# Kernel tuning notes

Measured on AMD Instinct MI355X. Metric: run time of the kernel, lower is better.

Reference implementation:

```python
import jax, jax.numpy as jnp
import numpy as np

NUM_DIHEDRALS = 3
# Idealized backbone geometry (picometers / radians), as in RGN/pNeRF.
BOND_LENGTHS = np.array([145.801, 152.326, 132.868], dtype=np.float32)  # N-CA, CA-C, C-N
BOND_ANGLES = np.array([2.124, 1.941, 2.028], dtype=np.float32)


def setup_inputs() -> dict:
    key = jax.random.key(0)
    num_steps, batch = 2048, 512
    flat_dihedrals = jax.random.uniform(
        key, (num_steps * batch, NUM_DIHEDRALS),
        minval=-np.pi, maxval=np.pi, dtype=jnp.float32)
    return {"flat_dihedrals": flat_dihedrals, "batch_size": batch}


def _l2_normalize(v, eps=1e-12):
    return v / jnp.sqrt(jnp.sum(v * v, axis=-1, keepdims=True) + eps)


def dihedral_to_point(dihedral):
    # dihedral: [L, B, 3] -> points in local frames: [3L, B, 3]
    r_cos_theta = np.float32(BOND_LENGTHS * np.cos(np.pi - BOND_ANGLES))  # [3]
    r_sin_theta = np.float32(BOND_LENGTHS * np.sin(np.pi - BOND_ANGLES))  # [3]
    L, B, _ = dihedral.shape
    pt_x = jnp.broadcast_to(jnp.asarray(r_cos_theta), (L, B, NUM_DIHEDRALS))
    pt_y = jnp.cos(dihedral) * r_sin_theta
    pt_z = jnp.sin(dihedral) * r_sin_theta
    point = jnp.stack([pt_x, pt_y, pt_z], axis=-1)      # [L, B, 3, 3]
    return point.reshape(L * NUM_DIHEDRALS, B, 3)       # [3L, B, 3]


def point_to_coordinate(points):
    # points: [N, B, 3]; sequential NeRF rigid-body chain extension.
    B = points.shape[1]
    init = np.array([[-np.sqrt(0.5), np.sqrt(1.5), 0.0],
                     [-np.sqrt(2.0), 0.0, 0.0],
                     [0.0, 0.0, 0.0]], dtype=np.float32)
    a = jnp.broadcast_to(jnp.asarray(init[0]), (B, 3))
    b = jnp.broadcast_to(jnp.asarray(init[1]), (B, 3))
    c = jnp.broadcast_to(jnp.asarray(init[2]), (B, 3))

    def step(carry, p):
        a, b, c = carry
        bc = _l2_normalize(c - b)                      # [B, 3]
        n = _l2_normalize(jnp.cross(b - a, bc))        # [B, 3]
        # Rotation matrix with columns [bc, n x bc, n]
        m = jnp.stack([bc, jnp.cross(n, bc), n], axis=-1)   # [B, 3, 3]
        coord = jnp.einsum('bij,bj->bi', m, p) + c          # [B, 3]
        return (b, c, coord), coord

    _, coords = jax.lax.scan(step, (a, b, c), points)
    return coords  # [N, B, 3]


def reference(flat_dihedrals, batch_size):
    num_steps = flat_dihedrals.shape[0] // batch_size
    dihedrals = flat_dihedrals.reshape(num_steps, batch_size, NUM_DIHEDRALS)
    points = dihedral_to_point(dihedrals)
    coordinates = point_to_coordinate(points)
    return coordinates
```

## Files before the change

kernel.cpp:

```cpp
#include <hip/hip_runtime.h>
#include <math.h>

#define BATCH 512
#define FRAGS 256
#define GROUP 16
#define NGRP  (FRAGS/GROUP)
#define BTILE 32
#define NTILE (BATCH/BTILE)
#define RPF   8
#define READY 0x5EADBEEF

__device__ __forceinline__ void compose(const float* A, const float* B, float* D) {
    float d[12];
    #pragma unroll
    for (int i = 0; i < 3; ++i) {
        #pragma unroll
        for (int j = 0; j < 3; ++j)
            d[i*3+j] = A[i*3+0]*B[0*3+j] + A[i*3+1]*B[1*3+j] + A[i*3+2]*B[2*3+j];
        d[9+i] = A[i*3+0]*B[9] + A[i*3+1]*B[10] + A[i*3+2]*B[11] + A[9+i];
    }
    #pragma unroll
    for (int k = 0; k < 12; ++k) D[k] = d[k];
}

__device__ __forceinline__ void set_identity(float* D) {
    D[0]=1.f; D[1]=0.f; D[2]=0.f;
    D[3]=0.f; D[4]=1.f; D[5]=0.f;
    D[6]=0.f; D[7]=0.f; D[8]=1.f;
    D[9]=0.f; D[10]=0.f; D[11]=0.f;
}

__device__ __forceinline__ void frame_of(
    float ax, float ay, float az,
    float bx, float by, float bz,
    float cx, float cy, float cz,
    float* out )
{
    float bcx = cx - bx, bcy = cy - by, bcz = cz - bz;
    float inv = rsqrtf(bcx*bcx + bcy*bcy + bcz*bcz + 1e-12f);
    bcx *= inv; bcy *= inv; bcz *= inv;
    float bax = bx - ax, bay = by - ay, baz = bz - az;
    float nx = bay*bcz - baz*bcy;
    float ny = baz*bcx - bax*bcz;
    float nz = bax*bcy - bay*bcx;
    inv = rsqrtf(nx*nx + ny*ny + nz*nz + 1e-12f);
    nx *= inv; ny *= inv; nz *= inv;
    float mx = ny*bcz - nz*bcy;
    float my = nz*bcx - nx*bcz;
    float mz = nx*bcy - ny*bcx;
    out[0] = bcx; out[1] = mx; out[2] = nx;
    out[3] = bcy; out[4] = my; out[5] = ny;
    out[6] = bcz; out[7] = mz; out[8] = nz;
    out[9] = cx; out[10] = cy; out[11] = cz;
}

__device__ __forceinline__ void nerf_step(
    float ax, float ay, float az,
    float bx, float by, float bz,
    float cx, float cy, float cz,
    float px, float py, float pz,
    float& ox, float& oy, float& oz)
{
    float bcx = cx - bx, bcy = cy - by, bcz = cz - bz;
    float inv = rsqrtf(bcx*bcx + bcy*bcy + bcz*bcz + 1e-12f);
    bcx *= inv; bcy *= inv; bcz *= inv;
    float bax = bx - ax, bay = by - ay, baz = bz - az;
    float nx = bay*bcz - baz*bcy;
    float ny = baz*bcx - bax*bcz;
    float nz = bax*bcy - bay*bcx;
    inv = rsqrtf(nx*nx + ny*ny + nz*nz + 1e-12f);
    nx *= inv; ny *= inv; nz *= inv;
    float mx = ny*bcz - nz*bcy;
    float my = nz*bcx - nx*bcz;
    float mz = nx*bcy - ny*bcx;
    ox = bcx*px + mx*py + nx*pz + cx;
    oy = bcy*px + my*py + ny*pz + cy;
    oz = bcz*px + mz*py + nz*pz + cz;
}

__device__ __forceinline__ void lane_consts(int b, float* rcl, float* rsl) {
    const float PI = 3.14159265358979323846f;
    float rc[3], rs[3];
    rc[0] = 145.801f * cosf(PI - 2.124f); rs[0] = 145.801f * sinf(PI - 2.124f);
    rc[1] = 152.326f * cosf(PI - 1.941f); rs[1] = 152.326f * sinf(PI - 1.941f);
    rc[2] = 132.868f * cosf(PI - 2.028f); rs[2] = 132.868f * sinf(PI - 2.028f);
    const int d0 = b % 3, d1 = (b + 2) % 3, d2 = (b + 1) % 3;
    rcl[0] = rc[d0]; rcl[1] = rc[d1]; rcl[2] = rc[d2];
    rsl[0] = rs[d0]; rsl[1] = rs[d1]; rsl[2] = rs[d2];
}

__global__ void __launch_bounds__(GROUP * BTILE) coord_onepass(
    const float* __restrict__ dih, float* __restrict__ T,
    int* __restrict__ flags, float* __restrict__ out)
{
    const int btile = blockIdx.x & (NTILE - 1);
    const int g     = blockIdx.x >> 4;
    const int bsub  = threadIdx.x & (BTILE - 1);
    const int j     = threadIdx.x >> 5;
    const int f     = g * GROUP + j;
    const int b     = btile * BTILE + bsub;

    __shared__ float BufA[GROUP * BTILE * 13];
    __shared__ float BufB[GROUP * BTILE * 13];
    float* rowA = &BufA[(size_t)threadIdx.x * 13];
    float* rowB = &BufB[(size_t)threadIdx.x * 13];

    float rcl[3], rsl[3];
    lane_consts(b, rcl, rsl);

    float dd[3 * RPF];
    #pragma unroll
    for (int r = 0; r < RPF; ++r) {
        const float* src = dih + (size_t)(f * RPF + r) * (3 * BATCH) + b;
        dd[r*3 + 0] = __builtin_nontemporal_load(src);
        dd[r*3 + 1] = __builtin_nontemporal_load(src + BATCH);
        dd[r*3 + 2] = __builtin_nontemporal_load(src + 2 * BATCH);
    }

    float lx[3 * RPF], ly[3 * RPF], lz[3 * RPF];

    float ax = -0.70710678118654752f, ay = 1.22474487139158905f, az = 0.0f;
    float bx = -1.41421356237309505f, by = 0.0f, bz = 0.0f;
    float cx = 0.0f, cy = 0.0f, cz = 0.0f;

    #pragma unroll
    for (int r = 0; r < RPF; ++r) {
        #pragma unroll
        for (int k = 0; k < 3; ++k) {
            float sn, cs;
            __sincosf(dd[r*3 + k], &sn, &cs);
            float ox, oy, oz;
            nerf_step(ax, ay, az, bx, by, bz, cx, cy, cz,
                      rcl[k], cs * rsl[k], sn * rsl[k], ox, oy, oz);
            ax = bx; ay = by; az = bz;
            bx = cx; by = cy; bz = cz;
            cx = ox; cy = oy; cz = oz;
            lx[r*3 + k] = ox; ly[r*3 + k] = oy; lz[r*3 + k] = oz;
        }
    }

    float cur[12];
    frame_of(ax, ay, az, bx, by, bz, cx, cy, cz, cur);

    #pragma unroll
    for (int k = 0; k < 12; ++k) rowA[k] = cur[k];
    __syncthreads();
    if (j >= 1) compose(&BufA[(size_t)(threadIdx.x - 1*BTILE) * 13], cur, cur);

    #pragma unroll
    for (int k = 0; k < 12; ++k) rowB[k] = cur[k];
    __syncthreads();
    if (j >= 2) compose(&BufB[(size_t)(threadIdx.x - 2*BTILE) * 13], cur, cur);

    #pragma unroll
    for (int k = 0; k < 12; ++k) rowA[k] = cur[k];
    __syncthreads();
    if (j >= 4) compose(&BufA[(size_t)(threadIdx.x - 4*BTILE) * 13], cur, cur);

    #pragma unroll
    for (int k = 0; k < 12; ++k) rowB[k] = cur[k];
    __syncthreads();
    if (j >= 8) compose(&BufB[(size_t)(threadIdx.x - 8*BTILE) * 13], cur, cur);

    #pragma unroll
    for (int k = 0; k < 12; ++k) rowA[k] = cur[k];
    __syncthreads();

    float pprev[12];
    if (j > 0) {
        #pragma unroll
        for (int k = 0; k < 12; ++k)
            pprev[k] = BufA[(size_t)(threadIdx.x - BTILE) * 13 + k];
    }

    if (j == GROUP - 1 && g < NGRP - 1) {
        #pragma unroll
        for (int k = 0; k < 12; ++k)
            __hip_atomic_store(&T[((size_t)g * 12 + k) * BATCH + b], cur[k],
                               __ATOMIC_RELAXED, __HIP_MEMORY_SCOPE_AGENT);
        if (bsub == 0)
            __hip_atomic_store(&flags[g * NTILE + btile], READY,
                               __ATOMIC_RELEASE, __HIP_MEMORY_SCOPE_AGENT);
    }

    float G[12];
    if (g == 0) {
        if (j == 0) set_identity(G);
        else {
            #pragma unroll
            for (int k = 0; k < 12; ++k) G[k] = pprev[k];
        }
    } else {
        float cur2[12];
        if (j < g) {
            while (__hip_atomic_load(&flags[j * NTILE + btile],
                                     __ATOMIC_RELAXED, __HIP_MEMORY_SCOPE_AGENT)
                   != READY) {
                __builtin_amdgcn_s_sleep(1);
            }
            __builtin_amdgcn_fence(__ATOMIC_ACQUIRE, "agent");
            #pragma unroll
            for (int k = 0; k < 12; ++k)
                cur2[k] = __hip_atomic_load(&T[((size_t)j * 12 + k) * BATCH + b],
                                            __ATOMIC_RELAXED, __HIP_MEMORY_SCOPE_AGENT);
        } else {
            set_identity(cur2);
        }

        #pragma unroll
        for (int k = 0; k < 12; ++k) rowB[k] = cur2[k];
        __syncthreads();
        if (j >= 1) compose(&BufB[(size_t)(threadIdx.x - 1*BTILE) * 13], cur2, cur2);

        #pragma unroll
        for (int k = 0; k < 12; ++k) rowA[k] = cur2[k];
        __syncthreads();
        if (j >= 2) compose(&BufA[(size_t)(threadIdx.x - 2*BTILE) * 13], cur2, cur2);

        #pragma unroll
        for (int k = 0; k < 12; ++k) rowB[k] = cur2[k];
        __syncthreads();
        if (j >= 4) compose(&BufB[(size_t)(threadIdx.x - 4*BTILE) * 13], cur2, cur2);

        #pragma unroll
        for (int k = 0; k < 12; ++k) rowA[k] = cur2[k];
        __syncthreads();
        if (j >= 8) compose(&BufA[(size_t)(threadIdx.x - 8*BTILE) * 13], cur2, cur2);

        #pragma unroll
        for (int k = 0; k < 12; ++k) rowB[k] = cur2[k];
        __syncthreads();
        float E[12];
        #pragma unroll
        for (int k = 0; k < 12; ++k)
            E[k] = BufB[(size_t)((g - 1) * BTILE + bsub) * 13 + k];

        if (j == 0) {
            #pragma unroll
            for (int k = 0; k < 12; ++k) G[k] = E[k];
        } else {
            compose(E, pprev, G);
        }
    }

    #pragma unroll
    for (int q = 0; q < 3 * RPF; ++q) {
        float ox = lx[q], oy = ly[q], oz = lz[q];
        float gx = G[0]*ox + G[1]*oy + G[2]*oz + G[9];
        float gy = G[3]*ox + G[4]*oy + G[5]*oz + G[10];
        float gz = G[6]*ox + G[7]*oy + G[8]*oz + G[11];
        size_t n = (size_t)f * (3 * RPF) + q;
        float* dst = out + (n * BATCH + b) * 3;
        __builtin_nontemporal_store(gx, dst + 0);
        __builtin_nontemporal_store(gy, dst + 1);
        __builtin_nontemporal_store(gz, dst + 2);
    }
}

extern "C" void kernel_launch(void* const* d_in, const int* in_sizes, int n_in,
                              void* d_out, int out_size, void* d_ws, size_t ws_size,
                              hipStream_t stream) {
    const float* dih = (const float*)d_in[0];
    float* out = (float*)d_out;
    float* T = (float*)d_ws;
    int* flags = (int*)(T + (size_t)NGRP * 12 * BATCH);

    coord_onepass<<<dim3(NGRP * NTILE), dim3(GROUP * BTILE), 0, stream>>>(
        dih, T, flags, out);
    (void)ws_size; (void)n_in; (void)out_size; (void)in_sizes;
}
```

Measured before the change: 96.32 us.

## Split per-thread NeRF chain into two interleaved independent half-chains

Each thread's 24-step sequential NeRF chain is split into two independent 12-step chains, both started from the canonical initial frame, and their steps are interleaved to expose instruction-level parallelism. The second half's local coordinates are mapped into the first half's frame through an extra frame composition (H1∘H2 for the fragment transform, G∘H1 for output). This halves the serial dependency depth of the chain at the cost of two extra 3x4 compositions, more live registers, and slightly different floating-point rounding.

```diff
diff --git a/kernel.cpp b/kernel.cpp
--- a/kernel.cpp
+++ b/kernel.cpp
@@ -8,6 +8,8 @@
 #define BTILE 32
 #define NTILE (BATCH/BTILE)
 #define RPF   8
+#define NPTS  (3*RPF)
+#define HALF  (NPTS/2)
 #define READY 0x5EADBEEF
 
 __device__ __forceinline__ void compose(const float* A, const float* B, float* D) {
@@ -108,7 +110,7 @@
     float rcl[3], rsl[3];
     lane_consts(b, rcl, rsl);
 
-    float dd[3 * RPF];
+    float dd[NPTS];
     #pragma unroll
     for (int r = 0; r < RPF; ++r) {
         const float* src = dih + (size_t)(f * RPF + r) * (3 * BATCH) + b;
@@ -117,30 +119,46 @@
         dd[r*3 + 2] = __builtin_nontemporal_load(src + 2 * BATCH);
     }
 
-    float lx[3 * RPF], ly[3 * RPF], lz[3 * RPF];
-
-    float ax = -0.70710678118654752f, ay = 1.22474487139158905f, az = 0.0f;
-    float bx = -1.41421356237309505f, by = 0.0f, bz = 0.0f;
-    float cx = 0.0f, cy = 0.0f, cz = 0.0f;
-
-    #pragma unroll
-    for (int r = 0; r < RPF; ++r) {
-        #pragma unroll
-        for (int k = 0; k < 3; ++k) {
-            float sn, cs;
-            __sincosf(dd[r*3 + k], &sn, &cs);
-            float ox, oy, oz;
-            nerf_step(ax, ay, az, bx, by, bz, cx, cy, cz,
-                      rcl[k], cs * rsl[k], sn * rsl[k], ox, oy, oz);
-            ax = bx; ay = by; az = bz;
-            bx = cx; by = cy; bz = cz;
-            cx = ox; cy = oy; cz = oz;
-            lx[r*3 + k] = ox; ly[r*3 + k] = oy; lz[r*3 + k] = oz;
-        }
-    }
-
-    float cur[12];
-    frame_of(ax, ay, az, bx, by, bz, cx, cy, cz, cur);
+    float lx[NPTS], ly[NPTS], lz[NPTS];
+
+    const float IAX = -0.70710678118654752f, IAY = 1.22474487139158905f;
+    const float IBX = -1.41421356237309505f;
+
+    float a0x = IAX, a0y = IAY, a0z = 0.0f;
+    float b0x = IBX, b0y = 0.0f, b0z = 0.0f;
+    float c0x = 0.0f, c0y = 0.0f, c0z = 0.0f;
+    float a1x = IAX, a1y = IAY, a1z = 0.0f;
+    float b1x = IBX, b1y = 0.0f, b1z = 0.0f;
+    float c1x = 0.0f, c1y = 0.0f, c1z = 0.0f;
+
+    #pragma unroll
+    for (int q = 0; q < HALF; ++q) {
+        const int k = q - (q / 3) * 3;
+        float sn0, cs0, sn1, cs1;
+        __sincosf(dd[q],        &sn0, &cs0);
+        __sincosf(dd[HALF + q], &sn1, &cs1);
+        float ox, oy, oz;
+        nerf_step(a0x, a0y, a0z, b0x, b0y, b0z, c0x, c0y, c0z,
+                  rcl[k], cs0 * rsl[k], sn0 * rsl[k], ox, oy, oz);
+        a0x = b0x; a0y = b0y; a0z = b0z;
+        b0x = c0x; b0y = c0y; b0z = c0z;
+        c0x = ox;  c0y = oy;  c0z = oz;
+        lx[q] = ox; ly[q] = oy; lz[q] = oz;
+        nerf_step(a1x, a1y, a1z, b1x, b1y, b1z, c1x, c1y, c1z,
+                  rcl[k], cs1 * rsl[k], sn1 * rsl[k], ox, oy, oz);
+        a1x = b1x; a1y = b1y; a1z = b1z;
+        b1x = c1x; b1y = c1y; b1z = c1z;
+        c1x = ox;  c1y = oy;  c1z = oz;
+        lx[HALF + q] = ox; ly[HALF + q] = oy; lz[HALF + q] = oz;
+    }
+
+    float H1[12], cur[12];
+    frame_of(a0x, a0y, a0z, b0x, b0y, b0z, c0x, c0y, c0z, H1);
+    {
+        float H2[12];
+        frame_of(a1x, a1y, a1z, b1x, b1y, b1z, c1x, c1y, c1z, H2);
+        compose(H1, H2, cur);
+    }
 
     #pragma unroll
     for (int k = 0; k < 12; ++k) rowA[k] = cur[k];
@@ -243,13 +261,17 @@
         }
     }
 
-    #pragma unroll
-    for (int q = 0; q < 3 * RPF; ++q) {
+    float G1[12];
+    compose(G, H1, G1);
+
+    #pragma unroll
+    for (int q = 0; q < NPTS; ++q) {
+        const float* M = (q < HALF) ? G : G1;
         float ox = lx[q], oy = ly[q], oz = lz[q];
-        float gx = G[0]*ox + G[1]*oy + G[2]*oz + G[9];
-        float gy = G[3]*ox + G[4]*oy + G[5]*oz + G[10];
-        float gz = G[6]*ox + G[7]*oy + G[8]*oz + G[11];
-        size_t n = (size_t)f * (3 * RPF) + q;
+        float gx = M[0]*ox + M[1]*oy + M[2]*oz + M[9];
+        float gy = M[3]*ox + M[4]*oy + M[5]*oz + M[10];
+        float gz = M[6]*ox + M[7]*oy + M[8]*oz + M[11];
+        size_t n = (size_t)f * NPTS + q;
         float* dst = out + (n * BATCH + b) * 3;
         __builtin_nontemporal_store(gx, dst + 0);
         __builtin_nontemporal_store(gy, dst + 1);
```

Measured after the change: 96.93 us. About the same (+0.6%).
